# Kernel tuning notes

Measured on AMD Instinct MI355X. Metric: run time of the kernel, lower is better.

Reference implementation:

```python
import jax, jax.numpy as jnp
import numpy as np

N_EXPERTS, D_MODEL, D_FF, TOP_K, N_TOKENS = 8, 1024, 4096, 2, 8192

def _uniform_init(key, shape, fan_in):
    # matches torch init: gain = sqrt(1/3), std = gain/sqrt(fan_in), bound = sqrt(3)*std
    bound = np.sqrt(3.0) * np.sqrt(1.0 / 3.0) / np.sqrt(fan_in)
    return jax.random.uniform(key, shape, minval=-bound, maxval=bound, dtype=jnp.float32)

def setup_inputs() -> dict:
    key = jax.random.key(0)
    kx, ki, kw, k1, k2, k3 = jax.random.split(key, 6)
    x = jax.random.normal(kx, (N_TOKENS, D_MODEL), dtype=jnp.float32)
    expert_indices = jax.random.randint(ki, (N_TOKENS, TOP_K), 0, N_EXPERTS, dtype=jnp.int32)
    expert_weights = jax.random.uniform(kw, (N_TOKENS, TOP_K), dtype=jnp.float32)
    w1 = _uniform_init(k1, (N_EXPERTS, D_MODEL, D_FF), D_MODEL)
    w2 = _uniform_init(k2, (N_EXPERTS, D_MODEL, D_FF), D_MODEL)
    w3 = _uniform_init(k3, (N_EXPERTS, D_FF, D_MODEL), D_FF)
    return {"x": x, "expert_indices": expert_indices, "expert_weights": expert_weights,
            "w1": w1, "w2": w2, "w3": w3}

def reference(x, expert_indices, expert_weights, w1, w2, w3):
    # For each token t and routed expert e with routing weight p:
    #   out[t] += p * (silu(x[t] @ W1[e]) * (x[t] @ W2[e])) @ W3[e]
    # Loop over the small fixed expert set; compute each expert's SwiGLU FFN
    # densely over all tokens and combine with per-token routing weights
    # (mathematically identical to the sorted-dispatch grouped GEMM).
    n_experts = w1.shape[0]
    out = jnp.zeros_like(x)
    for e in range(n_experts):
        gate = x @ w1[e]                 # [N, d_ff]
        val = x @ w2[e]                  # [N, d_ff]
        y = (jax.nn.silu(gate) * val) @ w3[e]   # [N, d_model]
        # sum routing weights over top_k slots that picked expert e
        p = jnp.sum(jnp.where(expert_indices == e, expert_weights, 0.0), axis=1)
        out = out + p[:, None] * y
    return out
```

## Files before the change

kernel.cpp:

```cpp
#include <hip/hip_runtime.h>
#include <hip/hip_bf16.h>

typedef __attribute__((ext_vector_type(8))) short short8;
typedef __attribute__((ext_vector_type(4))) float f32x4;
typedef unsigned short u16;
typedef unsigned int u32;

#define NTOK   8192
#define DMODEL 1024
#define DFF    4096
#define NEXP   8
#define NPAIR  (NTOK * 2)
#define PADM   256
#define MT1    72
#define PPAD   (MT1 * PADM)

#define OFF_XB   0ull
#define OFF_W1T  (OFF_XB  + (size_t)NTOK * DMODEL * 2)
#define OFF_W2T  (OFF_W1T + (size_t)NEXP * DFF * DMODEL * 2)
#define OFF_W3T  (OFF_W2T + (size_t)NEXP * DFF * DMODEL * 2)
#define OFF_H    (OFF_W3T + (size_t)NEXP * DMODEL * DFF * 2)
#define OFF_TOK  (OFF_H   + (size_t)PPAD * DFF * 2)
#define OFF_WGT  (OFF_TOK + (size_t)PPAD * 4)
#define OFF_CNT  (OFF_WGT + (size_t)PPAD * 4)
#define OFF_CUR  (OFF_CNT + 64)
#define OFF_OFFP (OFF_CUR + 64)
#define WS_END   (OFF_OFFP + 64)

#define GLOAD16(gp, lp)                                                        \
  __builtin_amdgcn_global_load_lds(                                            \
      (const __attribute__((address_space(1))) u32*)(gp),                      \
      (__attribute__((address_space(3))) u32*)(lp), 16, 0, 0)

__device__ __forceinline__ u16 f2bu(float f) {
  __hip_bfloat16 b = __float2bfloat16(f);
  return __builtin_bit_cast(u16, b);
}


__global__ __launch_bounds__(256) void cvt_x_k(const float* __restrict__ x,
                                               u16* __restrict__ xb) {
  int i = blockIdx.x * 256 + threadIdx.x;
  float4 v = ((const float4*)x)[i];
  unsigned long long pk = (unsigned long long)f2bu(v.x) |
                          ((unsigned long long)f2bu(v.y) << 16) |
                          ((unsigned long long)f2bu(v.z) << 32) |
                          ((unsigned long long)f2bu(v.w) << 48);
  ((unsigned long long*)xb)[i] = pk;
}

__global__ __launch_bounds__(256) void tr_cvt_k(const float* __restrict__ src,
                                                u16* __restrict__ dst, int R, int C) {
  src += (size_t)blockIdx.z * R * C;
  dst += (size_t)blockIdx.z * R * C;
  int c0 = blockIdx.x * 64, r0 = blockIdx.y * 64;
  __shared__ float tile[64][65];
  int tid = threadIdx.x;
  int f4 = tid & 15, rr = tid >> 4;
#pragma unroll
  for (int p = 0; p < 4; ++p) {
    int r = rr + p * 16;
    float4 v = *(const float4*)(src + (size_t)(r0 + r) * C + c0 + f4 * 4);
    tile[r][f4 * 4 + 0] = v.x; tile[r][f4 * 4 + 1] = v.y;
    tile[r][f4 * 4 + 2] = v.z; tile[r][f4 * 4 + 3] = v.w;
  }
  __syncthreads();
  int ch = tid & 7, cc = tid >> 3;
#pragma unroll
  for (int p = 0; p < 2; ++p) {
    int c = cc + p * 32;
    short8 s;
#pragma unroll
    for (int j = 0; j < 8; ++j) s[j] = (short)f2bu(tile[ch * 8 + j][c]);
    *(short8*)(dst + (size_t)(c0 + c) * R + r0 + ch * 8) = s;
  }
}


__global__ __launch_bounds__(256) void count_k(const int* __restrict__ ei,
                                               int* __restrict__ cnt) {
  int i = blockIdx.x * 256 + threadIdx.x;
  atomicAdd(&cnt[ei[i]], 1);
}

__global__ void scan_k(const int* __restrict__ cnt, int* __restrict__ offp) {
  if (threadIdx.x == 0) {
    int a = 0;
#pragma unroll
    for (int e = 0; e < NEXP; ++e) { offp[e] = a; a += (cnt[e] + PADM - 1) & ~(PADM - 1); }
    offp[NEXP] = a;
  }
}

__global__ __launch_bounds__(256) void scatter_k(const int* __restrict__ ei,
                                                 const float* __restrict__ ew,
                                                 const int* __restrict__ offp,
                                                 int* __restrict__ cur,
                                                 int* __restrict__ tok,
                                                 float* __restrict__ wg) {
  int i = blockIdx.x * 256 + threadIdx.x;
  int e = ei[i];
  int p = offp[e] + atomicAdd(&cur[e], 1);
  tok[p] = i >> 1;
  wg[p] = ew[i];
}


#define S1_BUF 16384
#define S1_NK  32

__global__ __launch_bounds__(512, 2) void stage1_k(const u16* __restrict__ xb,
                                                   const u16* __restrict__ w1t,
                                                   const u16* __restrict__ w2t,
                                                   u16* __restrict__ h,
                                                   const int* __restrict__ tok,
                                                   const int* __restrict__ offp) {
  extern __shared__ __align__(16) u16 lds[];
  const int r0 = blockIdx.y * PADM;
  if (r0 >= offp[NEXP]) return;
  int e = 0;
#pragma unroll
  for (int q = 0; q < 7; ++q) e += (offp[e + 1] <= r0) ? 1 : 0;
  const int n0 = blockIdx.x * 128;
  const int tid = threadIdx.x;
  const int lane = tid & 63, w = tid >> 6;
  const int wm = w >> 2, wn = w & 3;

  const int sl = lane & 3, rl = lane >> 2;
  const u16* aga[2];
  int adb[2];
#pragma unroll
  for (int j = 0; j < 2; ++j) {
    int row = w * 32 + j * 16 + rl;
    int t = tok[r0 + row];
    aga[j] = xb + (size_t)t * DMODEL + ((sl ^ ((row >> 1) & 3)) << 3);
    adb[j] = (w * 32 + j * 16) * 32;
  }
  const u16* w1e = w1t + (size_t)e * DFF * DMODEL;
  const u16* w2e = w2t + (size_t)e * DFF * DMODEL;
  const u16* bg1; const u16* bg2;
  int bdb;
  {
    int row = w * 16 + rl;
    size_t ro = (size_t)(n0 + row) * DMODEL + ((sl ^ ((row >> 1) & 3)) << 3);
    bg1 = w1e + ro; bg2 = w2e + ro;
    bdb = (w * 16) * 32;
  }

  int aoff[8], boff[2];
  {
    int ks = lane >> 4;
#pragma unroll
    for (int mi = 0; mi < 8; ++mi) {
      int row = wm * 128 + mi * 16 + (lane & 15);
      aoff[mi] = row * 32 + ((ks ^ ((row >> 1) & 3)) << 3);
    }
#pragma unroll
    for (int ni = 0; ni < 2; ++ni) {
      int col = wn * 32 + ni * 16 + (lane & 15);
      boff[ni] = col * 32 + ((ks ^ ((col >> 1) & 3)) << 3);
    }
  }

  f32x4 accg[8][2], accv[8][2];
  const f32x4 zero = {0.f, 0.f, 0.f, 0.f};
#pragma unroll
  for (int mi = 0; mi < 8; ++mi)
#pragma unroll
    for (int ni = 0; ni < 2; ++ni) { accg[mi][ni] = zero; accv[mi][ni] = zero; }

#define S1_ISSUE(Q, KO)                                                        \
  do {                                                                         \
    GLOAD16(aga[0] + (KO), (Q) + adb[0]);                                      \
    GLOAD16(aga[1] + (KO), (Q) + adb[1]);                                      \
    GLOAD16(bg1 + (KO), (Q) + 8192 + bdb);                                     \
    GLOAD16(bg2 + (KO), (Q) + 12288 + bdb);                                    \
  } while (0)

  S1_ISSUE(lds, 0);
  S1_ISSUE(lds + S1_BUF, 32);
  asm volatile("s_waitcnt vmcnt(4)" ::: "memory");
  __builtin_amdgcn_s_barrier();
  __builtin_amdgcn_sched_barrier(0);

#define S1_STEP(P, KC, ISSUE)                                                  \
  {                                                                            \
    const u16* Ab  = lds + (P) * S1_BUF;                                       \
    const u16* B1b = Ab + 8192;                                                \
    const u16* B2b = Ab + 12288;                                               \
    short8 af[8], b1f[2], b2f[2];                                              \
    _Pragma("unroll") for (int mi = 0; mi < 8; ++mi)                           \
      af[mi] = *(const short8*)(Ab + aoff[mi]);                                \
    _Pragma("unroll") for (int ni = 0; ni < 2; ++ni) {                         \
      b1f[ni] = *(const short8*)(B1b + boff[ni]);                              \
      b2f[ni] = *(const short8*)(B2b + boff[ni]);                              \
    }                                                                          \
    if (ISSUE) S1_ISSUE(lds + (((P) + 2) % 3) * S1_BUF, ((KC) + 2) * 32);      \
    __builtin_amdgcn_s_setprio(1);                                             \
    _Pragma("unroll") for (int mi = 0; mi < 8; ++mi)                           \
      _Pragma("unroll") for (int ni = 0; ni < 2; ++ni) {                       \
        accg[mi][ni] = __builtin_amdgcn_mfma_f32_16x16x32_bf16(                \
            af[mi], b1f[ni], accg[mi][ni], 0, 0, 0);                           \
        accv[mi][ni] = __builtin_amdgcn_mfma_f32_16x16x32_bf16(                \
            af[mi], b2f[ni], accv[mi][ni], 0, 0, 0);                           \
      }                                                                        \
    __builtin_amdgcn_s_setprio(0);                                             \
    if (ISSUE) asm volatile("s_waitcnt vmcnt(4)" ::: "memory");                \
    else       asm volatile("s_waitcnt vmcnt(0)" ::: "memory");                \
    __builtin_amdgcn_s_barrier();                                              \
    __builtin_amdgcn_sched_barrier(0);                                         \
  }

  for (int kc = 0; kc < S1_NK - 2; kc += 3) {
    S1_STEP(0, kc, 1)
    S1_STEP(1, kc + 1, 1)
    S1_STEP(2, kc + 2, 1)
  }
  S1_STEP(0, S1_NK - 2, 0)
  S1_STEP(1, S1_NK - 1, 0)
#undef S1_STEP
#undef S1_ISSUE

  const int prow = r0 + wm * 128 + ((lane >> 4) << 2);
  const int pcol = n0 + wn * 32 + (lane & 15);
#pragma unroll
  for (int mi = 0; mi < 8; ++mi)
#pragma unroll
    for (int ni = 0; ni < 2; ++ni)
#pragma unroll
      for (int j = 0; j < 4; ++j) {
        float g = accg[mi][ni][j];
        float v = accv[mi][ni][j];
        float s = g / (1.f + __expf(-g));
        h[(size_t)(prow + mi * 16 + j) * DFF + (pcol + ni * 16)] = f2bu(s * v);
      }
}


#define S2_BUF 24576
#define S2_NK  64

__global__ __launch_bounds__(512, 2) void stage2_k(const u16* __restrict__ h,
                                                   const u16* __restrict__ w3t,
                                                   float* __restrict__ out,
                                                   const int* __restrict__ tok,
                                                   const float* __restrict__ wg,
                                                   const int* __restrict__ offp) {
  extern __shared__ __align__(16) u16 lds[];
  const int r0 = blockIdx.y * 256;
  if (r0 >= offp[NEXP]) return;
  int e = 0;
#pragma unroll
  for (int q = 0; q < 7; ++q) e += (offp[e + 1] <= r0) ? 1 : 0;
  const int n0 = blockIdx.x * 128;
  const int tid = threadIdx.x;
  const int lane = tid & 63, w = tid >> 6;
  const int wm = w >> 1, wn = w & 1;
  const int lr = lane >> 3, seg = lane & 7;

  const u16* aga[4];
  int adb[4];
#pragma unroll
  for (int j = 0; j < 4; ++j) {
    int row = w * 32 + j * 8 + lr;
    aga[j] = h + (size_t)(r0 + row) * DFF + ((seg ^ (row & 7)) << 3);
    adb[j] = (w * 32 + j * 8) * 64;
  }
  const u16* w3e = w3t + (size_t)e * DMODEL * DFF;
  const u16* bga[2];
  int bdb[2];
#pragma unroll
  for (int j = 0; j < 2; ++j) {
    int row = w * 16 + j * 8 + lr;
    bga[j] = w3e + (size_t)(n0 + row) * DFF + ((seg ^ (row & 7)) << 3);
    bdb[j] = (w * 16 + j * 8) * 64;
  }

  int aoff[4][2], boff[4][2];
  {
    int ks = lane >> 4;
#pragma unroll
    for (int mi = 0; mi < 4; ++mi)
#pragma unroll
      for (int kk = 0; kk < 2; ++kk) {
        int row = wm * 64 + mi * 16 + (lane & 15);
        aoff[mi][kk] = row * 64 + (((kk * 4 + ks) ^ (row & 7)) << 3);
      }
#pragma unroll
    for (int ni = 0; ni < 4; ++ni)
#pragma unroll
      for (int kk = 0; kk < 2; ++kk) {
        int col = wn * 64 + ni * 16 + (lane & 15);
        boff[ni][kk] = col * 64 + (((kk * 4 + ks) ^ (col & 7)) << 3);
      }
  }

  f32x4 acc[4][4];
  const f32x4 zero = {0.f, 0.f, 0.f, 0.f};
#pragma unroll
  for (int mi = 0; mi < 4; ++mi)
#pragma unroll
    for (int ni = 0; ni < 4; ++ni) acc[mi][ni] = zero;

#define S2_ISSUE(Q, KO)                                                        \
  do {                                                                         \
    GLOAD16(aga[0] + (KO), (Q) + adb[0]);                                      \
    GLOAD16(aga[1] + (KO), (Q) + adb[1]);                                      \
    GLOAD16(aga[2] + (KO), (Q) + adb[2]);                                      \
    GLOAD16(aga[3] + (KO), (Q) + adb[3]);                                      \
    GLOAD16(bga[0] + (KO), (Q) + 16384 + bdb[0]);                              \
    GLOAD16(bga[1] + (KO), (Q) + 16384 + bdb[1]);                              \
  } while (0)

  S2_ISSUE(lds, 0);
  S2_ISSUE(lds + S2_BUF, 64);
  asm volatile("s_waitcnt vmcnt(6)" ::: "memory");
  __builtin_amdgcn_s_barrier();
  __builtin_amdgcn_sched_barrier(0);

#define S2_STEP(P, KC, ISSUE)                                                  \
  {                                                                            \
    const u16* Ab = lds + (P) * S2_BUF;                                        \
    const u16* Bb = Ab + 16384;                                                \
    short8 af[4][2], bf[4][2];                                                 \
    _Pragma("unroll") for (int mi = 0; mi < 4; ++mi)                           \
      _Pragma("unroll") for (int kk = 0; kk < 2; ++kk)                         \
        af[mi][kk] = *(const short8*)(Ab + aoff[mi][kk]);                      \
    _Pragma("unroll") for (int ni = 0; ni < 4; ++ni)                           \
      _Pragma("unroll") for (int kk = 0; kk < 2; ++kk)                         \
        bf[ni][kk] = *(const short8*)(Bb + boff[ni][kk]);                      \
    if (ISSUE) S2_ISSUE(lds + (((P) + 2) % 3) * S2_BUF, ((KC) + 2) * 64);      \
    __builtin_amdgcn_s_setprio(1);                                             \
    _Pragma("unroll") for (int kk = 0; kk < 2; ++kk)                           \
      _Pragma("unroll") for (int mi = 0; mi < 4; ++mi)                         \
        _Pragma("unroll") for (int ni = 0; ni < 4; ++ni)                       \
          acc[mi][ni] = __builtin_amdgcn_mfma_f32_16x16x32_bf16(               \
              af[mi][kk], bf[ni][kk], acc[mi][ni], 0, 0, 0);                   \
    __builtin_amdgcn_s_setprio(0);                                             \
    if (ISSUE) asm volatile("s_waitcnt vmcnt(6)" ::: "memory");                \
    else       asm volatile("s_waitcnt vmcnt(0)" ::: "memory");                \
    __builtin_amdgcn_s_barrier();                                              \
    __builtin_amdgcn_sched_barrier(0);                                         \
  }

  for (int kc = 0; kc < S2_NK - 4; kc += 3) {
    S2_STEP(0, kc, 1)
    S2_STEP(1, kc + 1, 1)
    S2_STEP(2, kc + 2, 1)
  }
  S2_STEP(0, S2_NK - 4, 1)
  S2_STEP(1, S2_NK - 3, 1)
  S2_STEP(2, S2_NK - 2, 0)
  S2_STEP(0, S2_NK - 1, 0)
#undef S2_STEP
#undef S2_ISSUE

  const int prow = r0 + wm * 64 + ((lane >> 4) << 2);
  const int pcolb = n0 + wn * 64 + (lane & 15);
#pragma unroll
  for (int mi = 0; mi < 4; ++mi)
#pragma unroll
    for (int j = 0; j < 4; ++j) {
      int pos = prow + mi * 16 + j;
      float p = wg[pos];
      if (p != 0.f) {
        int t = tok[pos];
#pragma unroll
        for (int ni = 0; ni < 4; ++ni)
          atomicAdd(&out[(size_t)t * DMODEL + pcolb + ni * 16], p * acc[mi][ni][j]);
      }
    }
}


extern "C" void kernel_launch(void* const* d_in, const int* in_sizes, int n_in,
                              void* d_out, int out_size, void* d_ws, size_t ws_size,
                              hipStream_t stream) {
  (void)in_sizes; (void)n_in;
  const float* x  = (const float*)d_in[0];
  const int*   ei = (const int*)d_in[1];
  const float* ew = (const float*)d_in[2];
  const float* w1 = (const float*)d_in[3];
  const float* w2 = (const float*)d_in[4];
  const float* w3 = (const float*)d_in[5];
  float* out = (float*)d_out;
  char* ws = (char*)d_ws;

  hipMemsetAsync(out, 0, (size_t)out_size * sizeof(float), stream);
  if (ws_size < WS_END) return;

  u16* xb   = (u16*)(ws + OFF_XB);
  u16* w1t  = (u16*)(ws + OFF_W1T);
  u16* w2t  = (u16*)(ws + OFF_W2T);
  u16* w3t  = (u16*)(ws + OFF_W3T);
  u16* hb   = (u16*)(ws + OFF_H);
  int* tok  = (int*)(ws + OFF_TOK);
  float* wg = (float*)(ws + OFF_WGT);
  int* cnt  = (int*)(ws + OFF_CNT);
  int* cur  = (int*)(ws + OFF_CUR);
  int* offp = (int*)(ws + OFF_OFFP);

  hipMemsetAsync(ws + OFF_TOK, 0, (size_t)(WS_END - OFF_TOK), stream);

  hipFuncSetAttribute(reinterpret_cast<const void*>(stage1_k),
                      hipFuncAttributeMaxDynamicSharedMemorySize, 98304);
  hipFuncSetAttribute(reinterpret_cast<const void*>(stage2_k),
                      hipFuncAttributeMaxDynamicSharedMemorySize, 147456);

  cvt_x_k<<<dim3(NTOK * DMODEL / 4 / 256), 256, 0, stream>>>(x, xb);
  tr_cvt_k<<<dim3(DFF / 64, DMODEL / 64, NEXP), 256, 0, stream>>>(w1, w1t, DMODEL, DFF);
  tr_cvt_k<<<dim3(DFF / 64, DMODEL / 64, NEXP), 256, 0, stream>>>(w2, w2t, DMODEL, DFF);
  tr_cvt_k<<<dim3(DMODEL / 64, DFF / 64, NEXP), 256, 0, stream>>>(w3, w3t, DFF, DMODEL);
  count_k<<<dim3(NPAIR / 256), 256, 0, stream>>>(ei, cnt);
  scan_k<<<1, 64, 0, stream>>>(cnt, offp);
  scatter_k<<<dim3(NPAIR / 256), 256, 0, stream>>>(ei, ew, offp, cur, tok, wg);
  stage1_k<<<dim3(DFF / 128, MT1), 512, 98304, stream>>>(xb, w1t, w2t, hb, tok, offp);
  stage2_k<<<dim3(DMODEL / 128, PPAD / 256), 512, 147456, stream>>>(hb, w3t, out, tok, wg, offp);
}
```

Before: 820.3 us.

## Double K-tile depth in stage1 with double-buffered 64-wide LDS stages

Stage1 now loads 64-element K tiles into two LDS buffers instead of 32-element tiles into three, halving the number of barrier steps. The LDS swizzle is changed to an 8-segment XOR for the wider rows. Each step issues the next tile's loads up front and waits for them fully at its end. Dynamic LDS per block grows to 128KB, which may limit residency and reduces prefetch depth.

```diff
diff --git a/kernel.cpp b/kernel.cpp
--- a/kernel.cpp
+++ b/kernel.cpp
@@ -106,8 +106,8 @@
 }
 
 
-#define S1_BUF 16384
-#define S1_NK  32
+#define S1_BUF 32768
+#define S1_NK  16
 
 __global__ __launch_bounds__(512, 2) void stage1_k(const u16* __restrict__ xb,
                                                    const u16* __restrict__ w1t,
@@ -125,41 +125,46 @@
   const int tid = threadIdx.x;
   const int lane = tid & 63, w = tid >> 6;
   const int wm = w >> 2, wn = w & 3;
-
-  const int sl = lane & 3, rl = lane >> 2;
-  const u16* aga[2];
-  int adb[2];
-#pragma unroll
-  for (int j = 0; j < 2; ++j) {
-    int row = w * 32 + j * 16 + rl;
+  const int lr = lane >> 3, seg = lane & 7;
+
+  const u16* aga[4];
+  int adb[4];
+#pragma unroll
+  for (int j = 0; j < 4; ++j) {
+    int row = w * 32 + j * 8 + lr;
     int t = tok[r0 + row];
-    aga[j] = xb + (size_t)t * DMODEL + ((sl ^ ((row >> 1) & 3)) << 3);
-    adb[j] = (w * 32 + j * 16) * 32;
+    aga[j] = xb + (size_t)t * DMODEL + ((seg ^ (row & 7)) << 3);
+    adb[j] = (w * 32 + j * 8) * 64;
   }
   const u16* w1e = w1t + (size_t)e * DFF * DMODEL;
   const u16* w2e = w2t + (size_t)e * DFF * DMODEL;
-  const u16* bg1; const u16* bg2;
-  int bdb;
-  {
-    int row = w * 16 + rl;
-    size_t ro = (size_t)(n0 + row) * DMODEL + ((sl ^ ((row >> 1) & 3)) << 3);
-    bg1 = w1e + ro; bg2 = w2e + ro;
-    bdb = (w * 16) * 32;
-  }
-
-  int aoff[8], boff[2];
+  const u16* bg1[2]; const u16* bg2[2];
+  int bdb[2];
+#pragma unroll
+  for (int j = 0; j < 2; ++j) {
+    int row = w * 16 + j * 8 + lr;
+    size_t ro = (size_t)(n0 + row) * DMODEL + ((seg ^ (row & 7)) << 3);
+    bg1[j] = w1e + ro; bg2[j] = w2e + ro;
+    bdb[j] = (w * 16 + j * 8) * 64;
+  }
+
+  int aoff[8][2], boff[2][2];
   {
     int ks = lane >> 4;
 #pragma unroll
-    for (int mi = 0; mi < 8; ++mi) {
-      int row = wm * 128 + mi * 16 + (lane & 15);
-      aoff[mi] = row * 32 + ((ks ^ ((row >> 1) & 3)) << 3);
-    }
-#pragma unroll
-    for (int ni = 0; ni < 2; ++ni) {
-      int col = wn * 32 + ni * 16 + (lane & 15);
-      boff[ni] = col * 32 + ((ks ^ ((col >> 1) & 3)) << 3);
-    }
+    for (int mi = 0; mi < 8; ++mi)
+#pragma unroll
+      for (int kk = 0; kk < 2; ++kk) {
+        int row = wm * 128 + mi * 16 + (lane & 15);
+        aoff[mi][kk] = row * 64 + (((kk * 4 + ks) ^ (row & 7)) << 3);
+      }
+#pragma unroll
+    for (int ni = 0; ni < 2; ++ni)
+#pragma unroll
+      for (int kk = 0; kk < 2; ++kk) {
+        int col = wn * 32 + ni * 16 + (lane & 15);
+        boff[ni][kk] = col * 64 + (((kk * 4 + ks) ^ (col & 7)) << 3);
+      }
   }
 
   f32x4 accg[8][2], accv[8][2];
@@ -173,50 +178,53 @@
   do {                                                                         \
     GLOAD16(aga[0] + (KO), (Q) + adb[0]);                                      \
     GLOAD16(aga[1] + (KO), (Q) + adb[1]);                                      \
-    GLOAD16(bg1 + (KO), (Q) + 8192 + bdb);                                     \
-    GLOAD16(bg2 + (KO), (Q) + 12288 + bdb);                                    \
+    GLOAD16(aga[2] + (KO), (Q) + adb[2]);                                      \
+    GLOAD16(aga[3] + (KO), (Q) + adb[3]);                                      \
+    GLOAD16(bg1[0] + (KO), (Q) + 16384 + bdb[0]);                              \
+    GLOAD16(bg1[1] + (KO), (Q) + 16384 + bdb[1]);                              \
+    GLOAD16(bg2[0] + (KO), (Q) + 24576 + bdb[0]);                              \
+    GLOAD16(bg2[1] + (KO), (Q) + 24576 + bdb[1]);                              \
   } while (0)
 
   S1_ISSUE(lds, 0);
-  S1_ISSUE(lds + S1_BUF, 32);
-  asm volatile("s_waitcnt vmcnt(4)" ::: "memory");
+  asm volatile("s_waitcnt vmcnt(0)" ::: "memory");
   __builtin_amdgcn_s_barrier();
   __builtin_amdgcn_sched_barrier(0);
 
 #define S1_STEP(P, KC, ISSUE)                                                  \
   {                                                                            \
     const u16* Ab  = lds + (P) * S1_BUF;                                       \
-    const u16* B1b = Ab + 8192;                                                \
-    const u16* B2b = Ab + 12288;                                               \
-    short8 af[8], b1f[2], b2f[2];                                              \
-    _Pragma("unroll") for (int mi = 0; mi < 8; ++mi)                           \
-      af[mi] = *(const short8*)(Ab + aoff[mi]);                                \
-    _Pragma("unroll") for (int ni = 0; ni < 2; ++ni) {                         \
-      b1f[ni] = *(const short8*)(B1b + boff[ni]);                              \
-      b2f[ni] = *(const short8*)(B2b + boff[ni]);                              \
+    const u16* B1b = Ab + 16384;                                               \
+    const u16* B2b = Ab + 24576;                                               \
+    if (ISSUE) S1_ISSUE(lds + (1 - (P)) * S1_BUF, ((KC) + 1) * 64);            \
+    _Pragma("unroll") for (int kk = 0; kk < 2; ++kk) {                         \
+      short8 af[8], b1f[2], b2f[2];                                            \
+      _Pragma("unroll") for (int mi = 0; mi < 8; ++mi)                         \
+        af[mi] = *(const short8*)(Ab + aoff[mi][kk]);                          \
+      _Pragma("unroll") for (int ni = 0; ni < 2; ++ni) {                       \
+        b1f[ni] = *(const short8*)(B1b + boff[ni][kk]);                        \
+        b2f[ni] = *(const short8*)(B2b + boff[ni][kk]);                        \
+      }                                                                        \
+      __builtin_amdgcn_s_setprio(1);                                           \
+      _Pragma("unroll") for (int mi = 0; mi < 8; ++mi)                         \
+        _Pragma("unroll") for (int ni = 0; ni < 2; ++ni) {                     \
+          accg[mi][ni] = __builtin_amdgcn_mfma_f32_16x16x32_bf16(              \
+              af[mi], b1f[ni], accg[mi][ni], 0, 0, 0);                         \
+          accv[mi][ni] = __builtin_amdgcn_mfma_f32_16x16x32_bf16(              \
+              af[mi], b2f[ni], accv[mi][ni], 0, 0, 0);                         \
+        }                                                                      \
+      __builtin_amdgcn_s_setprio(0);                                           \
     }                                                                          \
-    if (ISSUE) S1_ISSUE(lds + (((P) + 2) % 3) * S1_BUF, ((KC) + 2) * 32);      \
-    __builtin_amdgcn_s_setprio(1);                                             \
-    _Pragma("unroll") for (int mi = 0; mi < 8; ++mi)                           \
-      _Pragma("unroll") for (int ni = 0; ni < 2; ++ni) {                       \
-        accg[mi][ni] = __builtin_amdgcn_mfma_f32_16x16x32_bf16(                \
-            af[mi], b1f[ni], accg[mi][ni], 0, 0, 0);                           \
-        accv[mi][ni] = __builtin_amdgcn_mfma_f32_16x16x32_bf16(                \
-            af[mi], b2f[ni], accv[mi][ni], 0, 0, 0);                           \
-      }                                                                        \
-    __builtin_amdgcn_s_setprio(0);                                             \
-    if (ISSUE) asm volatile("s_waitcnt vmcnt(4)" ::: "memory");                \
-    else       asm volatile("s_waitcnt vmcnt(0)" ::: "memory");                \
+    asm volatile("s_waitcnt vmcnt(0)" ::: "memory");                           \
     __builtin_amdgcn_s_barrier();                                              \
     __builtin_amdgcn_sched_barrier(0);                                         \
   }
 
-  for (int kc = 0; kc < S1_NK - 2; kc += 3) {
+  for (int kc = 0; kc < S1_NK - 2; kc += 2) {
     S1_STEP(0, kc, 1)
     S1_STEP(1, kc + 1, 1)
-    S1_STEP(2, kc + 2, 1)
-  }
-  S1_STEP(0, S1_NK - 2, 0)
+  }
+  S1_STEP(0, S1_NK - 2, 1)
   S1_STEP(1, S1_NK - 1, 0)
 #undef S1_STEP
 #undef S1_ISSUE
@@ -403,7 +411,7 @@
   hipMemsetAsync(ws + OFF_TOK, 0, (size_t)(WS_END - OFF_TOK), stream);
 
   hipFuncSetAttribute(reinterpret_cast<const void*>(stage1_k),
-                      hipFuncAttributeMaxDynamicSharedMemorySize, 98304);
+                      hipFuncAttributeMaxDynamicSharedMemorySize, 131072);
   hipFuncSetAttribute(reinterpret_cast<const void*>(stage2_k),
                       hipFuncAttributeMaxDynamicSharedMemorySize, 147456);
 
@@ -414,6 +422,6 @@
   count_k<<<dim3(NPAIR / 256), 256, 0, stream>>>(ei, cnt);
   scan_k<<<1, 64, 0, stream>>>(cnt, offp);
   scatter_k<<<dim3(NPAIR / 256), 256, 0, stream>>>(ei, ew, offp, cur, tok, wg);
-  stage1_k<<<dim3(DFF / 128, MT1), 512, 98304, stream>>>(xb, w1t, w2t, hb, tok, offp);
+  stage1_k<<<dim3(DFF / 128, MT1), 512, 131072, stream>>>(xb, w1t, w2t, hb, tok, offp);
   stage2_k<<<dim3(DMODEL / 128, PPAD / 256), 512, 147456, stream>>>(hb, w3t, out, tok, wg, offp);
 }
```

Result: slower. 840.0 us (+2.4%).

## Widen stage2 tile to 256x256 with K=32 steps and smaller LDS buffers

Applied to the files above, without the earlier changes.

Stage2 now computes a 256-row by 256-column output tile per block, up from 256 by 128, with 8x4 MFMA tiles per wave. It moves to a 32-wide K step with a new 4-segment XOR swizzle and cuts per-stage LDS from 48 KB to 32 KB, so 96 KB total. The aim is to double reuse of each A (h) tile, halve the number of stage2 blocks, and lower global traffic per FLOP. In exchange there are twice as many pipeline steps and barriers, more accumulator registers (128 floats per lane), and fewer blocks to fill the GPU.

```diff
diff --git a/kernel.cpp b/kernel.cpp
--- a/kernel.cpp
+++ b/kernel.cpp
@@ -237,8 +237,8 @@
 }
 
 
-#define S2_BUF 24576
-#define S2_NK  64
+#define S2_BUF 16384
+#define S2_NK  128
 
 __global__ __launch_bounds__(512, 2) void stage2_k(const u16* __restrict__ h,
                                                    const u16* __restrict__ w3t,
@@ -252,53 +252,49 @@
   int e = 0;
 #pragma unroll
   for (int q = 0; q < 7; ++q) e += (offp[e + 1] <= r0) ? 1 : 0;
-  const int n0 = blockIdx.x * 128;
+  const int n0 = blockIdx.x * 256;
   const int tid = threadIdx.x;
   const int lane = tid & 63, w = tid >> 6;
-  const int wm = w >> 1, wn = w & 1;
-  const int lr = lane >> 3, seg = lane & 7;
-
-  const u16* aga[4];
-  int adb[4];
-#pragma unroll
-  for (int j = 0; j < 4; ++j) {
-    int row = w * 32 + j * 8 + lr;
-    aga[j] = h + (size_t)(r0 + row) * DFF + ((seg ^ (row & 7)) << 3);
-    adb[j] = (w * 32 + j * 8) * 64;
+  const int wm = w >> 2, wn = w & 3;
+
+  const int sl = lane & 3, rl = lane >> 2;
+  const u16* aga[2];
+  int adb[2];
+#pragma unroll
+  for (int j = 0; j < 2; ++j) {
+    int row = w * 32 + j * 16 + rl;
+    aga[j] = h + (size_t)(r0 + row) * DFF + ((sl ^ ((row >> 1) & 3)) << 3);
+    adb[j] = (w * 32 + j * 16) * 32;
   }
   const u16* w3e = w3t + (size_t)e * DMODEL * DFF;
   const u16* bga[2];
   int bdb[2];
 #pragma unroll
   for (int j = 0; j < 2; ++j) {
-    int row = w * 16 + j * 8 + lr;
-    bga[j] = w3e + (size_t)(n0 + row) * DFF + ((seg ^ (row & 7)) << 3);
-    bdb[j] = (w * 16 + j * 8) * 64;
-  }
-
-  int aoff[4][2], boff[4][2];
+    int row = w * 32 + j * 16 + rl;
+    bga[j] = w3e + (size_t)(n0 + row) * DFF + ((sl ^ ((row >> 1) & 3)) << 3);
+    bdb[j] = 8192 + (w * 32 + j * 16) * 32;
+  }
+
+  int aoff[8], boff[4];
   {
     int ks = lane >> 4;
 #pragma unroll
-    for (int mi = 0; mi < 4; ++mi)
-#pragma unroll
-      for (int kk = 0; kk < 2; ++kk) {
-        int row = wm * 64 + mi * 16 + (lane & 15);
-        aoff[mi][kk] = row * 64 + (((kk * 4 + ks) ^ (row & 7)) << 3);
-      }
-#pragma unroll
-    for (int ni = 0; ni < 4; ++ni)
-#pragma unroll
-      for (int kk = 0; kk < 2; ++kk) {
-        int col = wn * 64 + ni * 16 + (lane & 15);
-        boff[ni][kk] = col * 64 + (((kk * 4 + ks) ^ (col & 7)) << 3);
-      }
-  }
-
-  f32x4 acc[4][4];
+    for (int mi = 0; mi < 8; ++mi) {
+      int row = wm * 128 + mi * 16 + (lane & 15);
+      aoff[mi] = row * 32 + ((ks ^ ((row >> 1) & 3)) << 3);
+    }
+#pragma unroll
+    for (int ni = 0; ni < 4; ++ni) {
+      int col = wn * 64 + ni * 16 + (lane & 15);
+      boff[ni] = 8192 + col * 32 + ((ks ^ ((col >> 1) & 3)) << 3);
+    }
+  }
+
+  f32x4 acc[8][4];
   const f32x4 zero = {0.f, 0.f, 0.f, 0.f};
 #pragma unroll
-  for (int mi = 0; mi < 4; ++mi)
+  for (int mi = 0; mi < 8; ++mi)
 #pragma unroll
     for (int ni = 0; ni < 4; ++ni) acc[mi][ni] = zero;
 
@@ -306,59 +302,51 @@
   do {                                                                         \
     GLOAD16(aga[0] + (KO), (Q) + adb[0]);                                      \
     GLOAD16(aga[1] + (KO), (Q) + adb[1]);                                      \
-    GLOAD16(aga[2] + (KO), (Q) + adb[2]);                                      \
-    GLOAD16(aga[3] + (KO), (Q) + adb[3]);                                      \
-    GLOAD16(bga[0] + (KO), (Q) + 16384 + bdb[0]);                              \
-    GLOAD16(bga[1] + (KO), (Q) + 16384 + bdb[1]);                              \
+    GLOAD16(bga[0] + (KO), (Q) + bdb[0]);                                      \
+    GLOAD16(bga[1] + (KO), (Q) + bdb[1]);                                      \
   } while (0)
 
   S2_ISSUE(lds, 0);
-  S2_ISSUE(lds + S2_BUF, 64);
-  asm volatile("s_waitcnt vmcnt(6)" ::: "memory");
+  S2_ISSUE(lds + S2_BUF, 32);
+  asm volatile("s_waitcnt vmcnt(4)" ::: "memory");
   __builtin_amdgcn_s_barrier();
   __builtin_amdgcn_sched_barrier(0);
 
 #define S2_STEP(P, KC, ISSUE)                                                  \
   {                                                                            \
-    const u16* Ab = lds + (P) * S2_BUF;                                        \
-    const u16* Bb = Ab + 16384;                                                \
-    short8 af[4][2], bf[4][2];                                                 \
-    _Pragma("unroll") for (int mi = 0; mi < 4; ++mi)                           \
-      _Pragma("unroll") for (int kk = 0; kk < 2; ++kk)                         \
-        af[mi][kk] = *(const short8*)(Ab + aoff[mi][kk]);                      \
+    const u16* Qb = lds + (P) * S2_BUF;                                        \
+    short8 af[8], bf[4];                                                       \
+    _Pragma("unroll") for (int mi = 0; mi < 8; ++mi)                           \
+      af[mi] = *(const short8*)(Qb + aoff[mi]);                                \
     _Pragma("unroll") for (int ni = 0; ni < 4; ++ni)                           \
-      _Pragma("unroll") for (int kk = 0; kk < 2; ++kk)                         \
-        bf[ni][kk] = *(const short8*)(Bb + boff[ni][kk]);                      \
-    if (ISSUE) S2_ISSUE(lds + (((P) + 2) % 3) * S2_BUF, ((KC) + 2) * 64);      \
+      bf[ni] = *(const short8*)(Qb + boff[ni]);                                \
+    if (ISSUE) S2_ISSUE(lds + (((P) + 2) % 3) * S2_BUF, ((KC) + 2) * 32);      \
     __builtin_amdgcn_s_setprio(1);                                             \
-    _Pragma("unroll") for (int kk = 0; kk < 2; ++kk)                           \
-      _Pragma("unroll") for (int mi = 0; mi < 4; ++mi)                         \
-        _Pragma("unroll") for (int ni = 0; ni < 4; ++ni)                       \
-          acc[mi][ni] = __builtin_amdgcn_mfma_f32_16x16x32_bf16(               \
-              af[mi][kk], bf[ni][kk], acc[mi][ni], 0, 0, 0);                   \
+    _Pragma("unroll") for (int mi = 0; mi < 8; ++mi)                           \
+      _Pragma("unroll") for (int ni = 0; ni < 4; ++ni)                         \
+        acc[mi][ni] = __builtin_amdgcn_mfma_f32_16x16x32_bf16(                 \
+            af[mi], bf[ni], acc[mi][ni], 0, 0, 0);                             \
     __builtin_amdgcn_s_setprio(0);                                             \
-    if (ISSUE) asm volatile("s_waitcnt vmcnt(6)" ::: "memory");                \
+    if (ISSUE) asm volatile("s_waitcnt vmcnt(4)" ::: "memory");                \
     else       asm volatile("s_waitcnt vmcnt(0)" ::: "memory");                \
     __builtin_amdgcn_s_barrier();                                              \
     __builtin_amdgcn_sched_barrier(0);                                         \
   }
 
-  for (int kc = 0; kc < S2_NK - 4; kc += 3) {
+  for (int kc = 0; kc < S2_NK - 2; kc += 3) {
     S2_STEP(0, kc, 1)
     S2_STEP(1, kc + 1, 1)
     S2_STEP(2, kc + 2, 1)
   }
-  S2_STEP(0, S2_NK - 4, 1)
-  S2_STEP(1, S2_NK - 3, 1)
-  S2_STEP(2, S2_NK - 2, 0)
-  S2_STEP(0, S2_NK - 1, 0)
+  S2_STEP(0, S2_NK - 2, 0)
+  S2_STEP(1, S2_NK - 1, 0)
 #undef S2_STEP
 #undef S2_ISSUE
 
-  const int prow = r0 + wm * 64 + ((lane >> 4) << 2);
+  const int prow = r0 + wm * 128 + ((lane >> 4) << 2);
   const int pcolb = n0 + wn * 64 + (lane & 15);
 #pragma unroll
-  for (int mi = 0; mi < 4; ++mi)
+  for (int mi = 0; mi < 8; ++mi)
 #pragma unroll
     for (int j = 0; j < 4; ++j) {
       int pos = prow + mi * 16 + j;
@@ -405,7 +393,7 @@
   hipFuncSetAttribute(reinterpret_cast<const void*>(stage1_k),
                       hipFuncAttributeMaxDynamicSharedMemorySize, 98304);
   hipFuncSetAttribute(reinterpret_cast<const void*>(stage2_k),
-                      hipFuncAttributeMaxDynamicSharedMemorySize, 147456);
+                      hipFuncAttributeMaxDynamicSharedMemorySize, 98304);
 
   cvt_x_k<<<dim3(NTOK * DMODEL / 4 / 256), 256, 0, stream>>>(x, xb);
   tr_cvt_k<<<dim3(DFF / 64, DMODEL / 64, NEXP), 256, 0, stream>>>(w1, w1t, DMODEL, DFF);
@@ -415,5 +403,5 @@
   scan_k<<<1, 64, 0, stream>>>(cnt, offp);
   scatter_k<<<dim3(NPAIR / 256), 256, 0, stream>>>(ei, ew, offp, cur, tok, wg);
   stage1_k<<<dim3(DFF / 128, MT1), 512, 98304, stream>>>(xb, w1t, w2t, hb, tok, offp);
-  stage2_k<<<dim3(DMODEL / 128, PPAD / 256), 512, 147456, stream>>>(hb, w3t, out, tok, wg, offp);
-}
+  stage2_k<<<dim3(DMODEL / 256, PPAD / 256), 512, 98304, stream>>>(hb, w3t, out, tok, wg, offp);
+}
```

Result: no change. 834.0 us (+1.7%).
